# Performance work log

Hardware: AMD Instinct MI355X
Metric: run time of the kernel (lower is better)

## Reference

```python
import jax, jax.numpy as jnp
import numpy as np

B, C, G, S, R = 8192, 4096, 16, 256, 512  # batch, in_channels, clusters, cluster_size, j_rank


def setup_inputs() -> dict:
    key = jax.random.key(0)
    kx, kw, kb, kp = jax.random.split(key, 4)
    x = jax.random.normal(kx, (B, C), dtype=jnp.float32)
    # per-cluster Linear weights [G, out=R, in=S] and biases [G, R]
    W = jax.random.normal(kw, (G, R, S), dtype=jnp.float32) * (1.0 / np.sqrt(S))
    b = jax.random.normal(kb, (G, R), dtype=jnp.float32) * 0.01
    # arrangements: non-contiguous channel clusters = random permutation split into G groups
    perm = jax.random.permutation(kp, C).reshape(G, S).astype(jnp.int32)
    return {"x": x, "W": W, "b": b, "perm": perm}


def reference(x, W, b, perm):
    # gather each cluster's channels: [B, G, S]
    xg = x[:, perm]
    # batched per-cluster linear (y = x_c @ W_c^T + b_c), then concat along dim 1
    out = jnp.einsum('bgs,grs->bgr', xg, W) + b  # [B, G, R]
    return out.reshape(x.shape[0], G * R)
```

## Files before the change

kernel.cpp:

```cpp
#include <hip/hip_runtime.h>

#define BB 8192
#define CC 4096
#define GG 16
#define SS 256
#define RR 512
#define NN (GG*RR)

typedef __bf16 bf16x8 __attribute__((ext_vector_type(8)));
typedef float  f32x4_t __attribute__((ext_vector_type(4)));

__device__ __forceinline__ void gld_lds16(const void* g, void* l){
  __builtin_amdgcn_global_load_lds((const __attribute__((address_space(1))) void*)g,
                                   (__attribute__((address_space(3))) void*)l, 16, 0, 0);
}

__global__ void __launch_bounds__(256) prep_kernel(
    const float* __restrict__ x, const int* __restrict__ perm,
    const float* __restrict__ W,
    unsigned short* __restrict__ xp, unsigned short* __restrict__ Wb)
{
  __shared__ float row[CC];
  const int tid = threadIdx.x;
  const int bid = blockIdx.x;
  if (bid < BB) {
    const size_t b = bid;
    const float4* xr = (const float4*)(x + b*CC);
    float4* rr = (float4*)row;
    #pragma unroll
    for (int c=0;c<4;++c) rr[c*256+tid] = xr[c*256+tid];
    __syncthreads();
    unsigned short* xo = xp + b*CC;
    #pragma unroll
    for (int c=0;c<2;++c){
      const int j0 = (((c<<8)+tid)<<3);
      const int4 p0 = *(const int4*)(perm + j0);
      const int4 p1 = *(const int4*)(perm + j0 + 4);
      bf16x8 v;
      v[0]=(__bf16)row[p0.x]; v[1]=(__bf16)row[p0.y];
      v[2]=(__bf16)row[p0.z]; v[3]=(__bf16)row[p0.w];
      v[4]=(__bf16)row[p1.x]; v[5]=(__bf16)row[p1.y];
      v[6]=(__bf16)row[p1.z]; v[7]=(__bf16)row[p1.w];
      *(bf16x8*)(xo + j0) = v;
    }
  } else {
    const int i = (((bid - BB)<<8) + tid)<<3;
    const float4 f0 = ((const float4*)(W+i))[0];
    const float4 f1 = ((const float4*)(W+i))[1];
    bf16x8 v;
    v[0]=(__bf16)f0.x; v[1]=(__bf16)f0.y; v[2]=(__bf16)f0.z; v[3]=(__bf16)f0.w;
    v[4]=(__bf16)f1.x; v[5]=(__bf16)f1.y; v[6]=(__bf16)f1.z; v[7]=(__bf16)f1.w;
    *(bf16x8*)(Wb+i) = v;
  }
}

__global__ void __launch_bounds__(256, 3) gemm_kernel(
    const unsigned short* __restrict__ xp, const unsigned short* __restrict__ Wb,
    const float* __restrict__ bias, float* __restrict__ out)
{
  __shared__ unsigned short lA[128*64];
  __shared__ unsigned short lB[128*64];
  const int tid  = threadIdx.x;
  const int lane = tid & 63;
  const int w    = tid >> 6;
  const int wr   = w >> 1;
  const int wc   = w & 1;
  const int l15  = lane & 15, lh = lane >> 4;

  const int bid   = blockIdx.x;
  const int xcd   = bid & 7;
  const int local = bid >> 3;
  const int bx    = (xcd << 3) + (local & 7);
  const int by    = local >> 3;

  const int m0 = by << 7;
  const int n0 = bx << 7;
  const int g  = bx >> 2;
  const size_t arow0 = (size_t)m0*CC + (size_t)g*SS;
  const size_t brow0 = (size_t)n0*SS;

  f32x4_t acc[4][4];
  #pragma unroll
  for (int i=0;i<4;++i)
    #pragma unroll
    for (int j=0;j<4;++j)
      acc[i][j] = (f32x4_t){0.f,0.f,0.f,0.f};

  #pragma unroll
  for (int t=0;t<4;++t){
    const int kk = t<<6;
    #pragma unroll
    for (int c=0;c<4;++c){
      const int i  = (c<<8) + tid;
      const int r  = i>>3;
      const int cs = ((i&7) ^ (r&7)) << 3;
      gld_lds16(xp + arow0 + (size_t)r*CC + kk + cs, &lA[i<<3]);
    }
    #pragma unroll
    for (int c=0;c<4;++c){
      const int i  = (c<<8) + tid;
      const int r  = i>>3;
      const int cs = ((i&7) ^ (r&7)) << 3;
      gld_lds16(Wb + brow0 + (size_t)r*SS + kk + cs, &lB[i<<3]);
    }
    __syncthreads();
    #pragma unroll
    for (int ks=0;ks<2;++ks){
      bf16x8 af[4], bfr[4];
      const int cc = (ks<<2) + lh;
      #pragma unroll
      for (int mi=0;mi<4;++mi){
        const int ar = (wr<<6)+(mi<<4)+l15;
        af[mi]  = *(const bf16x8*)&lA[ar*64 + ((cc ^ (ar&7))<<3)];
      }
      #pragma unroll
      for (int ni=0;ni<4;++ni){
        const int br = (wc<<6)+(ni<<4)+l15;
        bfr[ni] = *(const bf16x8*)&lB[br*64 + ((cc ^ (br&7))<<3)];
      }
      #pragma unroll
      for (int mi=0;mi<4;++mi)
        #pragma unroll
        for (int ni=0;ni<4;++ni)
          acc[mi][ni] = __builtin_amdgcn_mfma_f32_16x16x32_bf16(af[mi], bfr[ni], acc[mi][ni], 0,0,0);
    }
    __syncthreads();
  }

  #pragma unroll
  for (int ni=0;ni<4;++ni){
    const int col = n0 + (wc<<6) + (ni<<4) + l15;
    const float bv = bias[col];
    #pragma unroll
    for (int mi=0;mi<4;++mi){
      const int rb = m0 + (wr<<6) + (mi<<4) + (lh<<2);
      float* op = out + (size_t)rb*NN + col;
      #pragma unroll
      for (int r=0;r<4;++r)
        op[(size_t)r*NN] = acc[mi][ni][r] + bv;
    }
  }
}

extern "C" void kernel_launch(void* const* d_in, const int* in_sizes, int n_in,
                              void* d_out, int out_size, void* d_ws, size_t ws_size,
                              hipStream_t stream) {
  const float* x    = (const float*)d_in[0];
  const float* W    = (const float*)d_in[1];
  const float* bias = (const float*)d_in[2];
  const int*   perm = (const int*)d_in[3];
  float* out = (float*)d_out;

  unsigned short* xp = (unsigned short*)d_ws;
  unsigned short* Wb = (unsigned short*)((char*)d_ws + (size_t)BB*CC*2);

  const int wblocks = (GG*RR*SS)/(256*8);
  prep_kernel<<<dim3(BB + wblocks), dim3(256), 0, stream>>>(x, perm, W, xp, Wb);
  gemm_kernel<<<dim3(4096), dim3(256), 0, stream>>>(xp, Wb, bias, out);
}
```

Baseline: 120.4 us.

## Double-buffer LDS with K=32 stages and vmcnt-based prefetch pipeline

Splits the K=256 loop into eight 32-wide stages held in two LDS buffers. The next-but-one stage is prefetched with direct global-to-LDS loads while the current one is computed, using s_waitcnt vmcnt to wait only for the older stage. The aim is to hide global load latency that the old load-sync-compute loop exposed. LDS use stays the same, but the kernel now runs twice as many barriers and uses a new swizzle for the 32-wide rows, which may bring bank conflicts.

```diff
diff --git a/kernel.cpp b/kernel.cpp
--- a/kernel.cpp
+++ b/kernel.cpp
@@ -58,8 +58,8 @@
     const unsigned short* __restrict__ xp, const unsigned short* __restrict__ Wb,
     const float* __restrict__ bias, float* __restrict__ out)
 {
-  __shared__ unsigned short lA[128*64];
-  __shared__ unsigned short lB[128*64];
+  __shared__ unsigned short lA[2][128*32];
+  __shared__ unsigned short lB[2][128*32];
   const int tid  = threadIdx.x;
   const int lane = tid & 63;
   const int w    = tid >> 6;
@@ -86,45 +86,52 @@
     for (int j=0;j<4;++j)
       acc[i][j] = (f32x4_t){0.f,0.f,0.f,0.f};
 
-  #pragma unroll
-  for (int t=0;t<4;++t){
-    const int kk = t<<6;
+  auto STAGE = [&](int kk, int buf){
     #pragma unroll
-    for (int c=0;c<4;++c){
+    for (int c=0;c<2;++c){
       const int i  = (c<<8) + tid;
-      const int r  = i>>3;
-      const int cs = ((i&7) ^ (r&7)) << 3;
-      gld_lds16(xp + arow0 + (size_t)r*CC + kk + cs, &lA[i<<3]);
+      const int r  = i>>2;
+      const int cs = ((i&3) ^ ((r>>1)&3)) << 3;
+      gld_lds16(xp + arow0 + (size_t)r*CC + kk + cs, &lA[buf][i<<3]);
     }
     #pragma unroll
-    for (int c=0;c<4;++c){
+    for (int c=0;c<2;++c){
       const int i  = (c<<8) + tid;
-      const int r  = i>>3;
-      const int cs = ((i&7) ^ (r&7)) << 3;
-      gld_lds16(Wb + brow0 + (size_t)r*SS + kk + cs, &lB[i<<3]);
+      const int r  = i>>2;
+      const int cs = ((i&3) ^ ((r>>1)&3)) << 3;
+      gld_lds16(Wb + brow0 + (size_t)r*SS + kk + cs, &lB[buf][i<<3]);
     }
-    __syncthreads();
+  };
+
+  auto COMPUTE = [&](int buf){
+    bf16x8 af[4], bfr[4];
     #pragma unroll
-    for (int ks=0;ks<2;++ks){
-      bf16x8 af[4], bfr[4];
-      const int cc = (ks<<2) + lh;
+    for (int mi=0;mi<4;++mi){
+      const int ar = (wr<<6)+(mi<<4)+l15;
+      af[mi]  = *(const bf16x8*)&lA[buf][ar*32 + ((lh ^ ((ar>>1)&3))<<3)];
+    }
+    #pragma unroll
+    for (int ni=0;ni<4;++ni){
+      const int br = (wc<<6)+(ni<<4)+l15;
+      bfr[ni] = *(const bf16x8*)&lB[buf][br*32 + ((lh ^ ((br>>1)&3))<<3)];
+    }
+    #pragma unroll
+    for (int mi=0;mi<4;++mi)
       #pragma unroll
-      for (int mi=0;mi<4;++mi){
-        const int ar = (wr<<6)+(mi<<4)+l15;
-        af[mi]  = *(const bf16x8*)&lA[ar*64 + ((cc ^ (ar&7))<<3)];
-      }
-      #pragma unroll
-      for (int ni=0;ni<4;++ni){
-        const int br = (wc<<6)+(ni<<4)+l15;
-        bfr[ni] = *(const bf16x8*)&lB[br*64 + ((cc ^ (br&7))<<3)];
-      }
-      #pragma unroll
-      for (int mi=0;mi<4;++mi)
-        #pragma unroll
-        for (int ni=0;ni<4;++ni)
-          acc[mi][ni] = __builtin_amdgcn_mfma_f32_16x16x32_bf16(af[mi], bfr[ni], acc[mi][ni], 0,0,0);
-    }
-    __syncthreads();
+      for (int ni=0;ni<4;++ni)
+        acc[mi][ni] = __builtin_amdgcn_mfma_f32_16x16x32_bf16(af[mi], bfr[ni], acc[mi][ni], 0,0,0);
+  };
+
+  STAGE(0, 0);
+  STAGE(32, 1);
+  #pragma unroll
+  for (int t=0;t<8;++t){
+    if (t<7) asm volatile("s_waitcnt vmcnt(4)" ::: "memory");
+    else     asm volatile("s_waitcnt vmcnt(0)" ::: "memory");
+    __builtin_amdgcn_s_barrier();
+    COMPUTE(t&1);
+    __builtin_amdgcn_s_barrier();
+    if (t<6) STAGE((t+2)<<5, t&1);
   }
 
   #pragma unroll
```

Result: slower. 126.0 us (+4.6%).

## Load GEMM fragments directly from global into registers, dropping LDS staging

Applied to the files above, without the earlier changes.

Removes the LDS tiles and barriers from the GEMM. Each wave now loads its MFMA A/B fragments straight from global memory into registers, with a two-stage register double buffer so the next K-slice load overlaps the current MFMAs. Occupancy hint lowered from 3 to 2 waves per SIMD to make room for the extra registers. The risk is that operand data shared across the block's waves is fetched redundantly from global/L2, with less coalesced 16-byte per-lane accesses, in exchange for no LDS traffic or synchronisation.

```diff
diff --git a/kernel.cpp b/kernel.cpp
--- a/kernel.cpp
+++ b/kernel.cpp
@@ -54,12 +54,10 @@
   }
 }
 
-__global__ void __launch_bounds__(256, 3) gemm_kernel(
+__global__ void __launch_bounds__(256, 2) gemm_kernel(
     const unsigned short* __restrict__ xp, const unsigned short* __restrict__ Wb,
     const float* __restrict__ bias, float* __restrict__ out)
 {
-  __shared__ unsigned short lA[128*64];
-  __shared__ unsigned short lB[128*64];
   const int tid  = threadIdx.x;
   const int lane = tid & 63;
   const int w    = tid >> 6;
@@ -76,8 +74,9 @@
   const int m0 = by << 7;
   const int n0 = bx << 7;
   const int g  = bx >> 2;
-  const size_t arow0 = (size_t)m0*CC + (size_t)g*SS;
-  const size_t brow0 = (size_t)n0*SS;
+
+  const unsigned short* pA = xp + (size_t)(m0 + (wr<<6) + l15)*CC + g*SS + (lh<<3);
+  const unsigned short* pB = Wb + (size_t)(n0 + (wc<<6) + l15)*SS + (lh<<3);
 
   f32x4_t acc[4][4];
   #pragma unroll
@@ -86,45 +85,31 @@
     for (int j=0;j<4;++j)
       acc[i][j] = (f32x4_t){0.f,0.f,0.f,0.f};
 
+  auto LOADF = [&](bf16x8* af, bf16x8* bf, int t){
+    const int kk = t<<5;
+    #pragma unroll
+    for (int mi=0;mi<4;++mi)
+      af[mi] = *(const bf16x8*)(pA + (size_t)(mi<<4)*CC + kk);
+    #pragma unroll
+    for (int ni=0;ni<4;++ni)
+      bf[ni] = *(const bf16x8*)(pB + (ni<<4)*SS + kk);
+  };
+  auto MFMAF = [&](bf16x8* af, bf16x8* bf){
+    #pragma unroll
+    for (int mi=0;mi<4;++mi)
+      #pragma unroll
+      for (int ni=0;ni<4;++ni)
+        acc[mi][ni] = __builtin_amdgcn_mfma_f32_16x16x32_bf16(af[mi], bf[ni], acc[mi][ni], 0,0,0);
+  };
+
+  bf16x8 afA[4], bfA[4], afB[4], bfB[4];
+  LOADF(afA, bfA, 0);
   #pragma unroll
-  for (int t=0;t<4;++t){
-    const int kk = t<<6;
-    #pragma unroll
-    for (int c=0;c<4;++c){
-      const int i  = (c<<8) + tid;
-      const int r  = i>>3;
-      const int cs = ((i&7) ^ (r&7)) << 3;
-      gld_lds16(xp + arow0 + (size_t)r*CC + kk + cs, &lA[i<<3]);
-    }
-    #pragma unroll
-    for (int c=0;c<4;++c){
-      const int i  = (c<<8) + tid;
-      const int r  = i>>3;
-      const int cs = ((i&7) ^ (r&7)) << 3;
-      gld_lds16(Wb + brow0 + (size_t)r*SS + kk + cs, &lB[i<<3]);
-    }
-    __syncthreads();
-    #pragma unroll
-    for (int ks=0;ks<2;++ks){
-      bf16x8 af[4], bfr[4];
-      const int cc = (ks<<2) + lh;
-      #pragma unroll
-      for (int mi=0;mi<4;++mi){
-        const int ar = (wr<<6)+(mi<<4)+l15;
-        af[mi]  = *(const bf16x8*)&lA[ar*64 + ((cc ^ (ar&7))<<3)];
-      }
-      #pragma unroll
-      for (int ni=0;ni<4;++ni){
-        const int br = (wc<<6)+(ni<<4)+l15;
-        bfr[ni] = *(const bf16x8*)&lB[br*64 + ((cc ^ (br&7))<<3)];
-      }
-      #pragma unroll
-      for (int mi=0;mi<4;++mi)
-        #pragma unroll
-        for (int ni=0;ni<4;++ni)
-          acc[mi][ni] = __builtin_amdgcn_mfma_f32_16x16x32_bf16(af[mi], bfr[ni], acc[mi][ni], 0,0,0);
-    }
-    __syncthreads();
+  for (int t=0;t<8;t+=2){
+    if (t+1<8) LOADF(afB, bfB, t+1);
+    MFMAF(afA, bfA);
+    if (t+2<8) LOADF(afA, bfA, t+2);
+    MFMAF(afB, bfB);
   }
 
   #pragma unroll
```

New measurement: 183.2 us. 1.52x slower.

## Double-buffer A tiles in LDS and load B fragments directly into registers

Applied to the files above, without the earlier changes.

The GEMM now keeps two LDS buffers for the A (gathered x) tile and prefetches the next two k-steps ahead with manual vmcnt waits, so global loads overlap with MFMA work. The B (weight) operand no longer goes through LDS: each wave loads its MFMA fragments straight from global memory into registers, also two stages ahead. This removes the LDS round trip and a barrier for B, but adds register pressure (16 extra bf16x8 registers) against a 3-blocks-per-SM launch bound. It also relies on hand-counted vmcnt values being correct for the mix of LDS-direct and register loads.

```diff
diff --git a/kernel.cpp b/kernel.cpp
--- a/kernel.cpp
+++ b/kernel.cpp
@@ -58,8 +58,7 @@
     const unsigned short* __restrict__ xp, const unsigned short* __restrict__ Wb,
     const float* __restrict__ bias, float* __restrict__ out)
 {
-  __shared__ unsigned short lA[128*64];
-  __shared__ unsigned short lB[128*64];
+  __shared__ unsigned short lA[2][128*64];
   const int tid  = threadIdx.x;
   const int lane = tid & 63;
   const int w    = tid >> 6;
@@ -77,7 +76,8 @@
   const int n0 = bx << 7;
   const int g  = bx >> 2;
   const size_t arow0 = (size_t)m0*CC + (size_t)g*SS;
-  const size_t brow0 = (size_t)n0*SS;
+
+  const unsigned short* pBg = Wb + (size_t)(n0 + (wc<<6) + l15)*SS + (lh<<3);
 
   f32x4_t acc[4][4];
   #pragma unroll
@@ -86,45 +86,55 @@
     for (int j=0;j<4;++j)
       acc[i][j] = (f32x4_t){0.f,0.f,0.f,0.f};
 
-  #pragma unroll
-  for (int t=0;t<4;++t){
-    const int kk = t<<6;
+  auto STAGE_A = [&](int kk, int buf){
     #pragma unroll
     for (int c=0;c<4;++c){
       const int i  = (c<<8) + tid;
       const int r  = i>>3;
       const int cs = ((i&7) ^ (r&7)) << 3;
-      gld_lds16(xp + arow0 + (size_t)r*CC + kk + cs, &lA[i<<3]);
+      gld_lds16(xp + arow0 + (size_t)r*CC + kk + cs, &lA[buf][i<<3]);
     }
+  };
+  auto LOAD_B = [&](bf16x8* bb, int t){
+    const int kk = t<<6;
     #pragma unroll
-    for (int c=0;c<4;++c){
-      const int i  = (c<<8) + tid;
-      const int r  = i>>3;
-      const int cs = ((i&7) ^ (r&7)) << 3;
-      gld_lds16(Wb + brow0 + (size_t)r*SS + kk + cs, &lB[i<<3]);
-    }
-    __syncthreads();
+    for (int ks=0;ks<2;++ks)
+      #pragma unroll
+      for (int ni=0;ni<4;++ni)
+        bb[(ks<<2)+ni] = *(const bf16x8*)(pBg + (size_t)(ni<<4)*SS + kk + (ks<<5));
+  };
+  auto COMPUTE = [&](int buf, bf16x8* bb){
     #pragma unroll
     for (int ks=0;ks<2;++ks){
-      bf16x8 af[4], bfr[4];
+      bf16x8 af[4];
       const int cc = (ks<<2) + lh;
       #pragma unroll
       for (int mi=0;mi<4;++mi){
         const int ar = (wr<<6)+(mi<<4)+l15;
-        af[mi]  = *(const bf16x8*)&lA[ar*64 + ((cc ^ (ar&7))<<3)];
-      }
-      #pragma unroll
-      for (int ni=0;ni<4;++ni){
-        const int br = (wc<<6)+(ni<<4)+l15;
-        bfr[ni] = *(const bf16x8*)&lB[br*64 + ((cc ^ (br&7))<<3)];
+        af[mi]  = *(const bf16x8*)&lA[buf][ar*64 + ((cc ^ (ar&7))<<3)];
       }
       #pragma unroll
       for (int mi=0;mi<4;++mi)
         #pragma unroll
         for (int ni=0;ni<4;++ni)
-          acc[mi][ni] = __builtin_amdgcn_mfma_f32_16x16x32_bf16(af[mi], bfr[ni], acc[mi][ni], 0,0,0);
+          acc[mi][ni] = __builtin_amdgcn_mfma_f32_16x16x32_bf16(af[mi], bb[(ks<<2)+ni], acc[mi][ni], 0,0,0);
     }
-    __syncthreads();
+  };
+
+  bf16x8 bA[8], bB[8];
+  STAGE_A(0, 0);  LOAD_B(bA, 0);
+  STAGE_A(64, 1); LOAD_B(bB, 1);
+  #pragma unroll
+  for (int t=0;t<4;++t){
+    if (t<3) asm volatile("s_waitcnt vmcnt(12)" ::: "memory");
+    else     asm volatile("s_waitcnt vmcnt(0)"  ::: "memory");
+    __builtin_amdgcn_s_barrier();
+    if (t&1) COMPUTE(1, bB); else COMPUTE(0, bA);
+    __builtin_amdgcn_s_barrier();
+    if (t<2){
+      STAGE_A((t+2)<<6, t&1);
+      if (t&1) LOAD_B(bB, t+2); else LOAD_B(bA, t+2);
+    }
   }
 
   #pragma unroll
```

New measurement: 129.0 us. 1.07x slower.
